# Kernel optimization log

Hardware: AMD Instinct MI355X
Metric: run time of the kernel (lower is better)

The kernel has to match this reference:

```python
import jax, jax.numpy as jnp
import numpy as np

MAX_SHIFT = 15
EPS = 1e-8


def setup_inputs() -> dict:
    key = jax.random.key(0)
    k1, k2 = jax.random.split(key)
    B, T = 2048, 2048
    preds = jax.random.normal(k1, (B, T), dtype=jnp.float32)
    targets = jax.random.normal(k2, (B, T), dtype=jnp.float32)
    return {"preds": preds, "targets": targets}


def reference(preds, targets):
    # targets statistics (shared across shifts)
    tc = targets - jnp.mean(targets, axis=1, keepdims=True)          # [B, T]
    std_t = jnp.sqrt(jnp.sum(tc * tc, axis=1) + EPS)                 # [B]

    shifts = jnp.arange(-MAX_SHIFT, MAX_SHIFT + 1)                   # [S]

    def pearson_for_shift(s):
        ps = jnp.roll(preds, s, axis=1)                              # [B, T]
        pc = ps - jnp.mean(ps, axis=1, keepdims=True)
        std_p = jnp.sqrt(jnp.sum(pc * pc, axis=1) + EPS)             # [B]
        cov = jnp.sum(pc * tc, axis=1)                               # [B]
        return cov / (std_p * std_t)

    pearsons = jax.vmap(pearson_for_shift)(shifts)                   # [S, B]
    best = jnp.maximum(jnp.max(pearsons, axis=0), -1.0)              # [B], init -1
    return 1.0 - jnp.mean(best)
```

## Files before the change

### kernel.cpp

```cpp
#include <hip/hip_runtime.h>

#define TLEN 2048
#define BROWS 2048
#define NSHIFT 31
#define BLOCK 256
#define ROWSPB 4
#define EPSF 1e-8f

__device__ __forceinline__ int padidx12(int k) { return 12 * (k >> 3) + (k & 7); }

template<int CTRL, int RMASK, bool BC>
__device__ __forceinline__ float dpp_mov(float v, float old) {
    return __int_as_float(__builtin_amdgcn_update_dpp(
        __float_as_int(old), __float_as_int(v), CTRL, RMASK, 0xF, BC));
}
__device__ __forceinline__ float wave_sum_dpp(float v) {
    v += dpp_mov<0x111, 0xF, true>(v, 0.f);
    v += dpp_mov<0x112, 0xF, true>(v, 0.f);
    v += dpp_mov<0x114, 0xF, true>(v, 0.f);
    v += dpp_mov<0x118, 0xF, true>(v, 0.f);
    v += dpp_mov<0x142, 0xA, true>(v, 0.f);
    v += dpp_mov<0x143, 0xC, true>(v, 0.f);
    return v;
}
__device__ __forceinline__ float wave_max_dpp(float v) {
    v = fmaxf(v, dpp_mov<0x111, 0xF, false>(v, v));
    v = fmaxf(v, dpp_mov<0x112, 0xF, false>(v, v));
    v = fmaxf(v, dpp_mov<0x114, 0xF, false>(v, v));
    v = fmaxf(v, dpp_mov<0x118, 0xF, false>(v, v));
    v = fmaxf(v, dpp_mov<0x142, 0xA, false>(v, v));
    v = fmaxf(v, dpp_mov<0x143, 0xC, false>(v, v));
    return v;
}

__global__ void __launch_bounds__(BLOCK, 2)
pearson_rows_kernel(const float* __restrict__ preds,
                    const float* __restrict__ targets,
                    float* __restrict__ row_best)
{
    __shared__ float smem[3408];
    float* wsum  = smem + 3120;
    float* rbufs = smem + 3376;

    const int tid  = threadIdx.x;
    const int wave = tid >> 6;
    const int lane = tid & 63;
    const int row0 = blockIdx.x * ROWSPB;

    const bool haloL = (tid < 4);
    const bool haloR = (tid >= 32 && tid < 36);
    {
    }
    const float* t0 = targets + (size_t)row0 * TLEN;
    const float* p0 = preds   + (size_t)row0 * TLEN;
    float4 tv0 = ((const float4*)t0)[tid];
    float4 tv1 = ((const float4*)t0)[tid + BLOCK];
    float4 hv  = make_float4(0.f, 0.f, 0.f, 0.f);
    if (haloL)      hv = *(const float4*)(t0 + 2032 + 4 * tid);
    else if (haloR) hv = *(const float4*)(t0 + 4 * (tid - 32));
    float4 pa = ((const float4*)p0)[2 * tid];
    float4 pb = ((const float4*)p0)[2 * tid + 1];

    #pragma unroll 1
    for (int it = 0; it < ROWSPB; ++it) {
        const int row = row0 + it;
        float* rbuf = rbufs + (it & 1) * 16;

        *(float4*)(smem + padidx12(4 * tid + 16))   = tv0;
        *(float4*)(smem + padidx12(4 * tid + 1040)) = tv1;
        if (haloL)      *(float4*)(smem + padidx12(4 * tid)) = hv;
        else if (haloR) *(float4*)(smem + padidx12(2064 + 4 * (tid - 32))) = hv;

        float4 ntv0 = tv0, ntv1 = tv1, nhv = hv, npa = pa, npb = pb;
        if (it + 1 < ROWSPB) {
            const float* nt = targets + (size_t)(row + 1) * TLEN;
            const float* np = preds   + (size_t)(row + 1) * TLEN;
            ntv0 = ((const float4*)nt)[tid];
            ntv1 = ((const float4*)nt)[tid + BLOCK];
            if (haloL)      nhv = *(const float4*)(nt + 2032 + 4 * tid);
            else if (haloR) nhv = *(const float4*)(nt + 4 * (tid - 32));
            npa = ((const float4*)np)[2 * tid];
            npb = ((const float4*)np)[2 * tid + 1];
        }

        float st  = (tv0.x + tv0.y) + (tv0.z + tv0.w) + (tv1.x + tv1.y) + (tv1.z + tv1.w);
        float stt = 0.f, sp = 0.f, spp = 0.f;
        stt = fmaf(tv0.x, tv0.x, stt); stt = fmaf(tv0.y, tv0.y, stt);
        stt = fmaf(tv0.z, tv0.z, stt); stt = fmaf(tv0.w, tv0.w, stt);
        stt = fmaf(tv1.x, tv1.x, stt); stt = fmaf(tv1.y, tv1.y, stt);
        stt = fmaf(tv1.z, tv1.z, stt); stt = fmaf(tv1.w, tv1.w, stt);
        sp  = (pa.x + pa.y) + (pa.z + pa.w) + (pb.x + pb.y) + (pb.z + pb.w);
        spp = fmaf(pa.x, pa.x, spp); spp = fmaf(pa.y, pa.y, spp);
        spp = fmaf(pa.z, pa.z, spp); spp = fmaf(pa.w, pa.w, spp);
        spp = fmaf(pb.x, pb.x, spp); spp = fmaf(pb.y, pb.y, spp);
        spp = fmaf(pb.z, pb.z, spp); spp = fmaf(pb.w, pb.w, spp);
        sp  = wave_sum_dpp(sp);
        spp = wave_sum_dpp(spp);
        st  = wave_sum_dpp(st);
        stt = wave_sum_dpp(stt);
        if (lane == 63) *(float4*)(rbuf + wave * 4) = make_float4(sp, spp, st, stt);
        __syncthreads();

        float w[40];
        {
            const float* g = smem + 12 * tid;
            #pragma unroll
            for (int q = 0; q < 5; ++q) {
                float4 a = *(const float4*)(g + 12 * q);
                float4 b = *(const float4*)(g + 12 * q + 4);
                w[8*q + 0] = a.x; w[8*q + 1] = a.y; w[8*q + 2] = a.z; w[8*q + 3] = a.w;
                w[8*q + 4] = b.x; w[8*q + 5] = b.y; w[8*q + 6] = b.z; w[8*q + 7] = b.w;
            }
            #pragma unroll
            for (int d = 1; d < 39; ++d) asm volatile("" : "+v"(w[d]));
        }

        float pc[8];
        pc[0] = pa.x; pc[1] = pa.y; pc[2] = pa.z; pc[3] = pa.w;
        pc[4] = pb.x; pc[5] = pb.y; pc[6] = pb.z; pc[7] = pb.w;
        float acc[NSHIFT];
        #pragma unroll
        for (int s = 0; s < NSHIFT; ++s) acc[s] = 0.f;
        #pragma unroll
        for (int m = 0; m < 8; ++m) {
            #pragma unroll
            for (int u = 0; u < NSHIFT; ++u)
                acc[u] = fmaf(pc[m], w[m + u + 1], acc[u]);
        }

        #pragma unroll
        for (int s = 0; s < NSHIFT; ++s) acc[s] = wave_sum_dpp(acc[s]);
        if (lane == 63) {
            float* dst = wsum + wave * 64;
            *(float4*)(dst +  0) = make_float4(acc[0],  acc[1],  acc[2],  acc[3]);
            *(float4*)(dst +  4) = make_float4(acc[4],  acc[5],  acc[6],  acc[7]);
            *(float4*)(dst +  8) = make_float4(acc[8],  acc[9],  acc[10], acc[11]);
            *(float4*)(dst + 12) = make_float4(acc[12], acc[13], acc[14], acc[15]);
            *(float4*)(dst + 16) = make_float4(acc[16], acc[17], acc[18], acc[19]);
            *(float4*)(dst + 20) = make_float4(acc[20], acc[21], acc[22], acc[23]);
            *(float4*)(dst + 24) = make_float4(acc[24], acc[25], acc[26], acc[27]);
            *(float2*)(dst + 28) = make_float2(acc[28], acc[29]);
            dst[30] = acc[30];
        }
        __syncthreads();

        if (wave == 0) {
            float dot = wsum[lane] + wsum[64 + lane] + wsum[128 + lane] + wsum[192 + lane];
            float4 r0 = *(const float4*)(rbuf + 0);
            float4 r1 = *(const float4*)(rbuf + 4);
            float4 r2 = *(const float4*)(rbuf + 8);
            float4 r3 = *(const float4*)(rbuf + 12);
            float SP  = r0.x + r1.x + r2.x + r3.x;
            float SPP = r0.y + r1.y + r2.y + r3.y;
            float ST  = r0.z + r1.z + r2.z + r3.z;
            float STT = r0.w + r1.w + r2.w + r3.w;
            const float invT = 1.0f / TLEN;
            float mp = SP * invT, mt = ST * invT;
            float varp = SPP - (float)TLEN * mp * mp;
            float vart = STT - (float)TLEN * mt * mt;
            float corr = (float)TLEN * mp * mt;
            float pear = (dot - corr) * rsqrtf((varp + EPSF) * (vart + EPSF));
            float v = (lane < NSHIFT) ? pear : -3.0e38f;
            v = wave_max_dpp(v);
            if (lane == 63) row_best[row] = fmaxf(v, -1.0f);
        }

        tv0 = ntv0; tv1 = ntv1; hv = nhv; pa = npa; pb = npb;
    }
}

__global__ void __launch_bounds__(BLOCK)
pearson_finalize_kernel(const float* __restrict__ row_best, float* __restrict__ out)
{
    __shared__ float r[4];
    const int tid = threadIdx.x, wave = tid >> 6, lane = tid & 63;
    float4 a = ((const float4*)row_best)[tid];
    float4 b = ((const float4*)row_best)[tid + BLOCK];
    float s = (a.x + a.y) + (a.z + a.w) + (b.x + b.y) + (b.z + b.w);
    s = wave_sum_dpp(s);
    if (lane == 63) r[wave] = s;
    __syncthreads();
    if (tid == 0)
        out[0] = 1.0f - (r[0] + r[1] + r[2] + r[3]) * (1.0f / (float)BROWS);
}

extern "C" void kernel_launch(void* const* d_in, const int* in_sizes, int n_in,
                              void* d_out, int out_size, void* d_ws, size_t ws_size,
                              hipStream_t stream) {
    const float* preds   = (const float*)d_in[0];
    const float* targets = (const float*)d_in[1];
    float* row_best = (float*)d_ws;
    float* out      = (float*)d_out;
    pearson_rows_kernel<<<BROWS / ROWSPB, BLOCK, 0, stream>>>(preds, targets, row_best);
    pearson_finalize_kernel<<<1, BLOCK, 0, stream>>>(row_best, out);
}
```

Before: 86.12 us.

## Process one row per block and raise occupancy hint to four blocks

```diff
diff --git a/kernel.cpp b/kernel.cpp
--- a/kernel.cpp
+++ b/kernel.cpp
@@ -4,7 +4,6 @@
 #define BROWS 2048
 #define NSHIFT 31
 #define BLOCK 256
-#define ROWSPB 4
 #define EPSF 1e-8f
 
 __device__ __forceinline__ int padidx12(int k) { return 12 * (k >> 3) + (k & 7); }
@@ -33,139 +32,117 @@
     return v;
 }
 
-__global__ void __launch_bounds__(BLOCK, 2)
+__global__ void __launch_bounds__(BLOCK, 4)
 pearson_rows_kernel(const float* __restrict__ preds,
                     const float* __restrict__ targets,
                     float* __restrict__ row_best)
 {
-    __shared__ float smem[3408];
-    float* wsum  = smem + 3120;
-    float* rbufs = smem + 3376;
+    __shared__ float smem[3392];
+    float* wsum = smem + 3120;
+    float* rbuf = smem + 3376;
 
     const int tid  = threadIdx.x;
     const int wave = tid >> 6;
     const int lane = tid & 63;
-    const int row0 = blockIdx.x * ROWSPB;
+    const int row  = blockIdx.x;
+    const float* p_row = preds   + (size_t)row * TLEN;
+    const float* t_row = targets + (size_t)row * TLEN;
 
+    float4 tv0 = ((const float4*)t_row)[tid];
+    float4 tv1 = ((const float4*)t_row)[tid + BLOCK];
+    float4 hv  = make_float4(0.f, 0.f, 0.f, 0.f);
     const bool haloL = (tid < 4);
     const bool haloR = (tid >= 32 && tid < 36);
+    if (haloL)      hv = *(const float4*)(t_row + 2032 + 4 * tid);
+    else if (haloR) hv = *(const float4*)(t_row + 4 * (tid - 32));
+    float4 pa = ((const float4*)p_row)[2 * tid];
+    float4 pb = ((const float4*)p_row)[2 * tid + 1];
+
+    *(float4*)(smem + padidx12(4 * tid + 16))   = tv0;
+    *(float4*)(smem + padidx12(4 * tid + 1040)) = tv1;
+    if (haloL)      *(float4*)(smem + padidx12(4 * tid)) = hv;
+    else if (haloR) *(float4*)(smem + padidx12(2064 + 4 * (tid - 32))) = hv;
+
+    float st  = (tv0.x + tv0.y) + (tv0.z + tv0.w) + (tv1.x + tv1.y) + (tv1.z + tv1.w);
+    float stt = 0.f, sp = 0.f, spp = 0.f;
+    stt = fmaf(tv0.x, tv0.x, stt); stt = fmaf(tv0.y, tv0.y, stt);
+    stt = fmaf(tv0.z, tv0.z, stt); stt = fmaf(tv0.w, tv0.w, stt);
+    stt = fmaf(tv1.x, tv1.x, stt); stt = fmaf(tv1.y, tv1.y, stt);
+    stt = fmaf(tv1.z, tv1.z, stt); stt = fmaf(tv1.w, tv1.w, stt);
+    sp  = (pa.x + pa.y) + (pa.z + pa.w) + (pb.x + pb.y) + (pb.z + pb.w);
+    spp = fmaf(pa.x, pa.x, spp); spp = fmaf(pa.y, pa.y, spp);
+    spp = fmaf(pa.z, pa.z, spp); spp = fmaf(pa.w, pa.w, spp);
+    spp = fmaf(pb.x, pb.x, spp); spp = fmaf(pb.y, pb.y, spp);
+    spp = fmaf(pb.z, pb.z, spp); spp = fmaf(pb.w, pb.w, spp);
+    sp  = wave_sum_dpp(sp);
+    spp = wave_sum_dpp(spp);
+    st  = wave_sum_dpp(st);
+    stt = wave_sum_dpp(stt);
+    if (lane == 63) *(float4*)(rbuf + wave * 4) = make_float4(sp, spp, st, stt);
+    __syncthreads();
+
+    float w[40];
     {
+        const float* g = smem + 12 * tid;
+        #pragma unroll
+        for (int q = 0; q < 5; ++q) {
+            float4 a = *(const float4*)(g + 12 * q);
+            float4 b = *(const float4*)(g + 12 * q + 4);
+            w[8*q + 0] = a.x; w[8*q + 1] = a.y; w[8*q + 2] = a.z; w[8*q + 3] = a.w;
+            w[8*q + 4] = b.x; w[8*q + 5] = b.y; w[8*q + 6] = b.z; w[8*q + 7] = b.w;
+        }
+        #pragma unroll
+        for (int d = 1; d < 39; ++d) asm volatile("" : "+v"(w[d]));
     }
-    const float* t0 = targets + (size_t)row0 * TLEN;
-    const float* p0 = preds   + (size_t)row0 * TLEN;
-    float4 tv0 = ((const float4*)t0)[tid];
-    float4 tv1 = ((const float4*)t0)[tid + BLOCK];
-    float4 hv  = make_float4(0.f, 0.f, 0.f, 0.f);
-    if (haloL)      hv = *(const float4*)(t0 + 2032 + 4 * tid);
-    else if (haloR) hv = *(const float4*)(t0 + 4 * (tid - 32));
-    float4 pa = ((const float4*)p0)[2 * tid];
-    float4 pb = ((const float4*)p0)[2 * tid + 1];
 
-    #pragma unroll 1
-    for (int it = 0; it < ROWSPB; ++it) {
-        const int row = row0 + it;
-        float* rbuf = rbufs + (it & 1) * 16;
+    float pc[8];
+    pc[0] = pa.x; pc[1] = pa.y; pc[2] = pa.z; pc[3] = pa.w;
+    pc[4] = pb.x; pc[5] = pb.y; pc[6] = pb.z; pc[7] = pb.w;
+    float acc[NSHIFT];
+    #pragma unroll
+    for (int s = 0; s < NSHIFT; ++s) acc[s] = 0.f;
+    #pragma unroll
+    for (int m = 0; m < 8; ++m) {
+        #pragma unroll
+        for (int u = 0; u < NSHIFT; ++u)
+            acc[u] = fmaf(pc[m], w[m + u + 1], acc[u]);
+    }
 
-        *(float4*)(smem + padidx12(4 * tid + 16))   = tv0;
-        *(float4*)(smem + padidx12(4 * tid + 1040)) = tv1;
-        if (haloL)      *(float4*)(smem + padidx12(4 * tid)) = hv;
-        else if (haloR) *(float4*)(smem + padidx12(2064 + 4 * (tid - 32))) = hv;
+    #pragma unroll
+    for (int s = 0; s < NSHIFT; ++s) acc[s] = wave_sum_dpp(acc[s]);
+    if (lane == 63) {
+        float* dst = wsum + wave * 64;
+        *(float4*)(dst +  0) = make_float4(acc[0],  acc[1],  acc[2],  acc[3]);
+        *(float4*)(dst +  4) = make_float4(acc[4],  acc[5],  acc[6],  acc[7]);
+        *(float4*)(dst +  8) = make_float4(acc[8],  acc[9],  acc[10], acc[11]);
+        *(float4*)(dst + 12) = make_float4(acc[12], acc[13], acc[14], acc[15]);
+        *(float4*)(dst + 16) = make_float4(acc[16], acc[17], acc[18], acc[19]);
+        *(float4*)(dst + 20) = make_float4(acc[20], acc[21], acc[22], acc[23]);
+        *(float4*)(dst + 24) = make_float4(acc[24], acc[25], acc[26], acc[27]);
+        *(float2*)(dst + 28) = make_float2(acc[28], acc[29]);
+        dst[30] = acc[30];
+    }
+    __syncthreads();
 
-        float4 ntv0 = tv0, ntv1 = tv1, nhv = hv, npa = pa, npb = pb;
-        if (it + 1 < ROWSPB) {
-            const float* nt = targets + (size_t)(row + 1) * TLEN;
-            const float* np = preds   + (size_t)(row + 1) * TLEN;
-            ntv0 = ((const float4*)nt)[tid];
-            ntv1 = ((const float4*)nt)[tid + BLOCK];
-            if (haloL)      nhv = *(const float4*)(nt + 2032 + 4 * tid);
-            else if (haloR) nhv = *(const float4*)(nt + 4 * (tid - 32));
-            npa = ((const float4*)np)[2 * tid];
-            npb = ((const float4*)np)[2 * tid + 1];
-        }
-
-        float st  = (tv0.x + tv0.y) + (tv0.z + tv0.w) + (tv1.x + tv1.y) + (tv1.z + tv1.w);
-        float stt = 0.f, sp = 0.f, spp = 0.f;
-        stt = fmaf(tv0.x, tv0.x, stt); stt = fmaf(tv0.y, tv0.y, stt);
-        stt = fmaf(tv0.z, tv0.z, stt); stt = fmaf(tv0.w, tv0.w, stt);
-        stt = fmaf(tv1.x, tv1.x, stt); stt = fmaf(tv1.y, tv1.y, stt);
-        stt = fmaf(tv1.z, tv1.z, stt); stt = fmaf(tv1.w, tv1.w, stt);
-        sp  = (pa.x + pa.y) + (pa.z + pa.w) + (pb.x + pb.y) + (pb.z + pb.w);
-        spp = fmaf(pa.x, pa.x, spp); spp = fmaf(pa.y, pa.y, spp);
-        spp = fmaf(pa.z, pa.z, spp); spp = fmaf(pa.w, pa.w, spp);
-        spp = fmaf(pb.x, pb.x, spp); spp = fmaf(pb.y, pb.y, spp);
-        spp = fmaf(pb.z, pb.z, spp); spp = fmaf(pb.w, pb.w, spp);
-        sp  = wave_sum_dpp(sp);
-        spp = wave_sum_dpp(spp);
-        st  = wave_sum_dpp(st);
-        stt = wave_sum_dpp(stt);
-        if (lane == 63) *(float4*)(rbuf + wave * 4) = make_float4(sp, spp, st, stt);
-        __syncthreads();
-
-        float w[40];
-        {
-            const float* g = smem + 12 * tid;
-            #pragma unroll
-            for (int q = 0; q < 5; ++q) {
-                float4 a = *(const float4*)(g + 12 * q);
-                float4 b = *(const float4*)(g + 12 * q + 4);
-                w[8*q + 0] = a.x; w[8*q + 1] = a.y; w[8*q + 2] = a.z; w[8*q + 3] = a.w;
-                w[8*q + 4] = b.x; w[8*q + 5] = b.y; w[8*q + 6] = b.z; w[8*q + 7] = b.w;
-            }
-            #pragma unroll
-            for (int d = 1; d < 39; ++d) asm volatile("" : "+v"(w[d]));
-        }
-
-        float pc[8];
-        pc[0] = pa.x; pc[1] = pa.y; pc[2] = pa.z; pc[3] = pa.w;
-        pc[4] = pb.x; pc[5] = pb.y; pc[6] = pb.z; pc[7] = pb.w;
-        float acc[NSHIFT];
-        #pragma unroll
-        for (int s = 0; s < NSHIFT; ++s) acc[s] = 0.f;
-        #pragma unroll
-        for (int m = 0; m < 8; ++m) {
-            #pragma unroll
-            for (int u = 0; u < NSHIFT; ++u)
-                acc[u] = fmaf(pc[m], w[m + u + 1], acc[u]);
-        }
-
-        #pragma unroll
-        for (int s = 0; s < NSHIFT; ++s) acc[s] = wave_sum_dpp(acc[s]);
-        if (lane == 63) {
-            float* dst = wsum + wave * 64;
-            *(float4*)(dst +  0) = make_float4(acc[0],  acc[1],  acc[2],  acc[3]);
-            *(float4*)(dst +  4) = make_float4(acc[4],  acc[5],  acc[6],  acc[7]);
-            *(float4*)(dst +  8) = make_float4(acc[8],  acc[9],  acc[10], acc[11]);
-            *(float4*)(dst + 12) = make_float4(acc[12], acc[13], acc[14], acc[15]);
-            *(float4*)(dst + 16) = make_float4(acc[16], acc[17], acc[18], acc[19]);
-            *(float4*)(dst + 20) = make_float4(acc[20], acc[21], acc[22], acc[23]);
-            *(float4*)(dst + 24) = make_float4(acc[24], acc[25], acc[26], acc[27]);
-            *(float2*)(dst + 28) = make_float2(acc[28], acc[29]);
-            dst[30] = acc[30];
-        }
-        __syncthreads();
-
-        if (wave == 0) {
-            float dot = wsum[lane] + wsum[64 + lane] + wsum[128 + lane] + wsum[192 + lane];
-            float4 r0 = *(const float4*)(rbuf + 0);
-            float4 r1 = *(const float4*)(rbuf + 4);
-            float4 r2 = *(const float4*)(rbuf + 8);
-            float4 r3 = *(const float4*)(rbuf + 12);
-            float SP  = r0.x + r1.x + r2.x + r3.x;
-            float SPP = r0.y + r1.y + r2.y + r3.y;
-            float ST  = r0.z + r1.z + r2.z + r3.z;
-            float STT = r0.w + r1.w + r2.w + r3.w;
-            const float invT = 1.0f / TLEN;
-            float mp = SP * invT, mt = ST * invT;
-            float varp = SPP - (float)TLEN * mp * mp;
-            float vart = STT - (float)TLEN * mt * mt;
-            float corr = (float)TLEN * mp * mt;
-            float pear = (dot - corr) * rsqrtf((varp + EPSF) * (vart + EPSF));
-            float v = (lane < NSHIFT) ? pear : -3.0e38f;
-            v = wave_max_dpp(v);
-            if (lane == 63) row_best[row] = fmaxf(v, -1.0f);
-        }
-
-        tv0 = ntv0; tv1 = ntv1; hv = nhv; pa = npa; pb = npb;
+    if (wave == 0) {
+        float dot = wsum[lane] + wsum[64 + lane] + wsum[128 + lane] + wsum[192 + lane];
+        float4 r0 = *(const float4*)(rbuf + 0);
+        float4 r1 = *(const float4*)(rbuf + 4);
+        float4 r2 = *(const float4*)(rbuf + 8);
+        float4 r3 = *(const float4*)(rbuf + 12);
+        float SP  = r0.x + r1.x + r2.x + r3.x;
+        float SPP = r0.y + r1.y + r2.y + r3.y;
+        float ST  = r0.z + r1.z + r2.z + r3.z;
+        float STT = r0.w + r1.w + r2.w + r3.w;
+        const float invT = 1.0f / TLEN;
+        float mp = SP * invT, mt = ST * invT;
+        float varp = SPP - (float)TLEN * mp * mp;
+        float vart = STT - (float)TLEN * mt * mt;
+        float corr = (float)TLEN * mp * mt;
+        float pear = (dot - corr) * rsqrtf((varp + EPSF) * (vart + EPSF));
+        float v = (lane < NSHIFT) ? pear : -3.0e38f;
+        v = wave_max_dpp(v);
+        if (lane == 63) row_best[row] = fmaxf(v, -1.0f);
     }
 }
 
@@ -191,6 +168,6 @@
     const float* targets = (const float*)d_in[1];
     float* row_best = (float*)d_ws;
     float* out      = (float*)d_out;
-    pearson_rows_kernel<<<BROWS / ROWSPB, BLOCK, 0, stream>>>(preds, targets, row_best);
+    pearson_rows_kernel<<<BROWS, BLOCK, 0, stream>>>(preds, targets, row_best);
     pearson_finalize_kernel<<<1, BLOCK, 0, stream>>>(row_best, out);
 }
```

New measurement: 81.79 us. 1.05x faster.
